# Performance work log

Measured on AMD Instinct MI355X. Metric: run time of the kernel, lower is better.

Reference implementation:

```python
import jax, jax.numpy as jnp
import numpy as np

B, N, E = 64, 20000, 160000
F_TEXT, HID, OUT = 300, 1024, 1664
NEG_SLOPE = 0.2


def setup_inputs() -> dict:
    key = jax.random.key(0)
    ks = jax.random.split(key, 9)
    img_feat = jax.random.normal(ks[0], (B, OUT), dtype=jnp.float32)
    node_features = jax.random.normal(ks[1], (N, F_TEXT), dtype=jnp.float32)
    edge_src = jax.random.randint(ks[2], (E,), 0, N, dtype=jnp.int32)
    edge_dst = jax.random.randint(ks[3], (E,), 0, N, dtype=jnp.int32)
    edge_weight = jax.random.uniform(ks[4], (E,), dtype=jnp.float32)
    W1 = jax.random.normal(ks[5], (F_TEXT, HID), dtype=jnp.float32) / np.sqrt(F_TEXT)
    b1 = jax.random.normal(ks[6], (HID,), dtype=jnp.float32) * 0.01
    W2 = jax.random.normal(ks[7], (HID, OUT), dtype=jnp.float32) / np.sqrt(HID)
    b2 = jax.random.normal(ks[8], (OUT,), dtype=jnp.float32) * 0.01
    return {"img_feat": img_feat, "node_features": node_features,
            "edge_src": edge_src, "edge_dst": edge_dst, "edge_weight": edge_weight,
            "W1": W1, "b1": b1, "W2": W2, "b2": b2}


def _gcn_norm(edge_src, edge_dst, edge_weight, num_nodes):
    # PyG gcn_norm with add_self_loops=False: symmetric degree normalization
    deg = jax.ops.segment_sum(edge_weight, edge_dst, num_segments=num_nodes)
    dinv = jnp.where(deg > 0, jax.lax.rsqrt(deg), 0.0)
    return dinv[edge_src] * edge_weight * dinv[edge_dst]


def _gcn_conv(x, edge_src, edge_dst, norm, W, b):
    # GCNConv: linear transform, then normalized gather -> scatter-add, then bias
    h = x @ W  # [N, out]
    msgs = h[edge_src] * norm[:, None]  # [E, out] gather + scale
    agg = jax.ops.segment_sum(msgs, edge_dst, num_segments=x.shape[0])
    return agg + b


def reference(img_feat, node_features, edge_src, edge_dst, edge_weight, W1, b1, W2, b2):
    num_nodes = node_features.shape[0]
    norm = _gcn_norm(edge_src, edge_dst, edge_weight, num_nodes)
    x = _gcn_conv(node_features, edge_src, edge_dst, norm, W1, b1)
    x = jnp.where(x >= 0, x, NEG_SLOPE * x)  # leaky_relu(0.2)
    x = _gcn_conv(x, edge_src, edge_dst, norm, W2, b2)
    return img_feat @ x.T  # [B, N]
```

## Files before the change

kernel.cpp:

```cpp
#include <hip/hip_runtime.h>
#include <hip/hip_bf16.h>

#define NNODES 20000
#define NEDGES 160000
#define BQ     64
#define FTEXT  300
#define KPAD1  320
#define HIDDIM 1024
#define OUTDIM 1664

typedef __attribute__((ext_vector_type(8))) short short8;
typedef __attribute__((ext_vector_type(4))) float floatx4;

__device__ inline unsigned short f2bf(float f) {
    union { float f; unsigned int u; } v; v.f = f;
    unsigned int r = v.u + 0x7FFF + ((v.u >> 16) & 1);
    return (unsigned short)(r >> 16);
}
__device__ inline float bf2f(unsigned short h) {
    union { unsigned int u; float f; } v; v.u = ((unsigned int)h) << 16;
    return v.f;
}

__global__ void degcnt_kernel(const int* __restrict__ dst, const float* __restrict__ w,
                              float* __restrict__ deg, int* __restrict__ cnt, int E) {
    int e = blockIdx.x * blockDim.x + threadIdx.x;
    if (e < E) {
        int d = dst[e];
        atomicAdd(&deg[d], w[e]);
        atomicAdd(&cnt[d], 1);
    }
}

__global__ __launch_bounds__(1024) void scan_kernel(const int* __restrict__ cnt,
                                                    int* __restrict__ row_start, int N) {
    __shared__ int partial[1024];
    const int CH = 20;
    int t = threadIdx.x;
    int begin = t * CH;
    int nloc = N - begin; if (nloc > CH) nloc = CH; if (nloc < 0) nloc = 0;
    int vals[CH];
    int s = 0;
    if (nloc == CH) {
        #pragma unroll
        for (int i = 0; i < CH / 4; i++) {
            int4 v = ((const int4*)(cnt + begin))[i];
            vals[i*4+0] = v.x; vals[i*4+1] = v.y; vals[i*4+2] = v.z; vals[i*4+3] = v.w;
            s += v.x + v.y + v.z + v.w;
        }
    } else {
        for (int i = 0; i < nloc; i++) { vals[i] = cnt[begin + i]; s += vals[i]; }
    }
    partial[t] = s;
    __syncthreads();
    for (int off = 1; off < 1024; off <<= 1) {
        int v = (t >= off) ? partial[t - off] : 0;
        __syncthreads();
        partial[t] += v;
        __syncthreads();
    }
    int run = (t == 0) ? 0 : partial[t - 1];
    for (int i = 0; i < nloc; i++) { row_start[begin + i] = run; run += vals[i]; }
    if (t == 1023) row_start[N] = partial[1023];
}

__global__ void fill_kernel(const int* __restrict__ dst, const int* __restrict__ src,
                            const float* __restrict__ w, const float* __restrict__ deg,
                            const int* __restrict__ row_start, int* __restrict__ cursor,
                            int* __restrict__ src_s, float* __restrict__ wnrm_s, int E) {
    int e = blockIdx.x * blockDim.x + threadIdx.x;
    if (e < E) {
        int d = dst[e], s = src[e];
        float dd = deg[d], ds = deg[s];
        float nv = (ds > 0.f ? rsqrtf(ds) : 0.f) * w[e] * (dd > 0.f ? rsqrtf(dd) : 0.f);
        int pos = row_start[d] + atomicAdd(&cursor[d], 1);
        src_s[pos] = s;
        wnrm_s[pos] = nv;
    }
}

__global__ __launch_bounds__(256) void aggnf_kernel(const unsigned short* __restrict__ nfb,
        const int* __restrict__ row_start, const int* __restrict__ src_s,
        const float* __restrict__ wnrm_s, unsigned short* __restrict__ out) {
    int wave = threadIdx.x >> 6, lane = threadIdx.x & 63;
    int d = blockIdx.x * 4 + wave;
    int s0 = row_start[d], s1 = row_start[d + 1];
    float4 acc  = make_float4(0.f, 0.f, 0.f, 0.f);
    float4 acc2 = make_float4(0.f, 0.f, 0.f, 0.f);
    for (int base = s0; base < s1; base += 64) {
        int m = s1 - base; if (m > 64) m = 64;
        int   src_l = (lane < m) ? src_s[base + lane]  : 0;
        float w_l   = (lane < m) ? wnrm_s[base + lane] : 0.f;
        int sj = __shfl(src_l, 0);
        float wj = __shfl(w_l, 0);
        const ushort4* row = (const ushort4*)(nfb + (long)sj * FTEXT);
        ushort4 hv  = row[lane];
        ushort4 hv2 = make_ushort4(0, 0, 0, 0);
        if (lane < 11) hv2 = row[64 + lane];
        for (int j = 0; j < m; j++) {
            ushort4 nv  = make_ushort4(0, 0, 0, 0);
            ushort4 nv2 = make_ushort4(0, 0, 0, 0);
            float wn = 0.f;
            if (j + 1 < m) {
                int sn = __shfl(src_l, j + 1);
                wn = __shfl(w_l, j + 1);
                const ushort4* nrow = (const ushort4*)(nfb + (long)sn * FTEXT);
                nv = nrow[lane];
                if (lane < 11) nv2 = nrow[64 + lane];
            }
            acc.x  += bf2f(hv.x)  * wj; acc.y  += bf2f(hv.y)  * wj;
            acc.z  += bf2f(hv.z)  * wj; acc.w  += bf2f(hv.w)  * wj;
            acc2.x += bf2f(hv2.x) * wj; acc2.y += bf2f(hv2.y) * wj;
            acc2.z += bf2f(hv2.z) * wj; acc2.w += bf2f(hv2.w) * wj;
            hv = nv; hv2 = nv2; wj = wn;
        }
    }
    unsigned short* orow = out + (long)d * KPAD1;
    ushort4 o;
    o.x = f2bf(acc.x); o.y = f2bf(acc.y); o.z = f2bf(acc.z); o.w = f2bf(acc.w);
    ((ushort4*)orow)[lane] = o;
    if (lane < 16) {
        ushort4 o2 = make_ushort4(0, 0, 0, 0);
        if (lane < 11) {
            o2.x = f2bf(acc2.x); o2.y = f2bf(acc2.y);
            o2.z = f2bf(acc2.z); o2.w = f2bf(acc2.w);
        }
        ((ushort4*)orow)[64 + lane] = o2;
    }
}

#define W1N  (HIDDIM * KPAD1)
#define N1F4 (HIDDIM * OUTDIM / 4)
#define N2F4 (BQ * OUTDIM / 4)
#define N3F4 (NNODES * FTEXT / 4)
__global__ void cvt_all_kernel(const float* __restrict__ W1, unsigned short* __restrict__ W1bt,
                               const float* __restrict__ W2, unsigned short* __restrict__ W2b,
                               const float* __restrict__ img, unsigned short* __restrict__ imgb,
                               const float* __restrict__ nf, unsigned short* __restrict__ nfb) {
    int i = blockIdx.x * 256 + threadIdx.x;
    if (i < W1N) {
        int n = i / KPAD1, k = i % KPAD1;
        float v = (k < FTEXT) ? W1[(long)k * HIDDIM + n] : 0.f;
        W1bt[i] = f2bf(v);
        return;
    }
    i -= W1N;
    const float* in; unsigned short* outp; int j;
    if (i < N1F4)                    { in = W2;  outp = W2b;  j = i; }
    else if (i < N1F4 + N2F4)        { in = img; outp = imgb; j = i - N1F4; }
    else if (i < N1F4 + N2F4 + N3F4) { in = nf;  outp = nfb;  j = i - N1F4 - N2F4; }
    else return;
    float4 v = ((const float4*)in)[j];
    ushort4 o;
    o.x = f2bf(v.x); o.y = f2bf(v.y); o.z = f2bf(v.z); o.w = f2bf(v.w);
    ((ushort4*)outp)[j] = o;
}

__global__ __launch_bounds__(256) void ztcvec_kernel(const float* __restrict__ Ztf,
        unsigned short* __restrict__ Zt, const float* __restrict__ img,
        const float* __restrict__ b2, float* __restrict__ cvec) {
    if (blockIdx.x < (BQ * HIDDIM) / 256) {
        int i = blockIdx.x * 256 + threadIdx.x;
        Zt[i] = f2bf(Ztf[i]);
    } else {
        int b = blockIdx.x - (BQ * HIDDIM) / 256;
        int l = threadIdx.x;
        float v = 0.f;
        for (int f = l; f < OUTDIM; f += 256) v += img[(long)b * OUTDIM + f] * b2[f];
        __shared__ float red[256];
        red[l] = v;
        __syncthreads();
        if (l < 64) {
            v = red[l] + red[l + 64] + red[l + 128] + red[l + 192];
            for (int off = 32; off > 0; off >>= 1) v += __shfl_down(v, off);
            if (l == 0) cvec[b] = v;
        }
    }
}

template<int EPI, int OUT_BF16, int ATOMIC, int NT>
__global__ __launch_bounds__(256) void mfma_gemm(
        const unsigned short* __restrict__ A, const unsigned short* __restrict__ B,
        const float* __restrict__ bias, void* __restrict__ Cv,
        int M, int N, int K, int ldc) {
    constexpr int CT = NT / 16;
    __shared__ unsigned short As[128][40];
    __shared__ unsigned short Bs[NT][40];
    int t = threadIdx.x;
    int m0 = blockIdx.y * 128;
    int n0 = blockIdx.x * NT;
    int klen = K / gridDim.z;
    int kbeg = blockIdx.z * klen;
    int wave = t >> 6, lane = t & 63;
    int lm = lane & 15, lq = lane >> 4;
    floatx4 acc[2][CT] = {};
    for (int k0 = kbeg; k0 < kbeg + klen; k0 += 32) {
        #pragma unroll
        for (int p = 0; p < 2; p++) {
            int idx = p * 256 + t;
            int r = idx >> 2, c8 = (idx & 3) * 8;
            uint4 v = make_uint4(0, 0, 0, 0);
            int gm = m0 + r;
            if (gm < M) v = *(const uint4*)(A + (long)gm * K + k0 + c8);
            *(uint4*)&As[r][c8] = v;
        }
        #pragma unroll
        for (int p = 0; p < NT / 64; p++) {
            int idx = p * 256 + t;
            int r = idx >> 2, c8 = (idx & 3) * 8;
            uint4 v = *(const uint4*)(B + (long)(n0 + r) * K + k0 + c8);
            *(uint4*)&Bs[r][c8] = v;
        }
        __syncthreads();
        short8 a[2], b[CT];
        #pragma unroll
        for (int rt = 0; rt < 2; rt++)
            a[rt] = *(const short8*)&As[wave * 32 + rt * 16 + lm][lq * 8];
        #pragma unroll
        for (int ct = 0; ct < CT; ct++)
            b[ct] = *(const short8*)&Bs[ct * 16 + lm][lq * 8];
        #pragma unroll
        for (int rt = 0; rt < 2; rt++)
            #pragma unroll
            for (int ct = 0; ct < CT; ct++)
                acc[rt][ct] = __builtin_amdgcn_mfma_f32_16x16x32_bf16(
                    a[rt], b[ct], acc[rt][ct], 0, 0, 0);
        __syncthreads();
    }
    #pragma unroll
    for (int rt = 0; rt < 2; rt++) {
        #pragma unroll
        for (int r = 0; r < 4; r++) {
            int gm = m0 + wave * 32 + rt * 16 + lq * 4 + r;
            if (gm >= M) continue;
            #pragma unroll
            for (int ct = 0; ct < CT; ct++) {
                int gn = n0 + ct * 16 + lm;
                float v = acc[rt][ct][r];
                if (EPI) { v += bias[gn]; v = v >= 0.f ? v : 0.2f * v; }
                if (OUT_BF16)      ((unsigned short*)Cv)[(long)gm * ldc + gn] = f2bf(v);
                else if (ATOMIC)   atomicAdd((float*)Cv + (long)gm * ldc + gn, v);
                else               ((float*)Cv)[(long)gm * ldc + gn] = v;
            }
        }
    }
}

__global__ __launch_bounds__(512) void xy_gemm(
        const unsigned short* __restrict__ aggNF, const unsigned short* __restrict__ W1bt,
        const float* __restrict__ b1, const unsigned short* __restrict__ Zt,
        float* __restrict__ Y, int M) {
    __shared__ unsigned short smem[128 * 136];
    unsigned short (*As)[40]  = (unsigned short (*)[40])smem;
    unsigned short (*Bs)[40]  = (unsigned short (*)[40])(smem + 5120);
    unsigned short (*xs)[136] = (unsigned short (*)[136])smem;
    int t = threadIdx.x;
    int wave = t >> 6, lane = t & 63;
    int lm = lane & 15, lq = lane >> 4;
    int m0 = blockIdx.y * 128;
    int n0 = blockIdx.x * 128;
    floatx4 acc[8] = {};
    for (int k0 = 0; k0 < KPAD1; k0 += 32) {
        {
            int r = t >> 2, c8 = (t & 3) * 8;
            uint4 v = make_uint4(0, 0, 0, 0);
            int gm = m0 + r;
            if (gm < M) v = *(const uint4*)(aggNF + (long)gm * KPAD1 + k0 + c8);
            *(uint4*)&As[r][c8] = v;
        }
        {
            int r = t >> 2, c8 = (t & 3) * 8;
            uint4 v = *(const uint4*)(W1bt + (long)(n0 + r) * KPAD1 + k0 + c8);
            *(uint4*)&Bs[r][c8] = v;
        }
        __syncthreads();
        short8 a = *(const short8*)&As[wave * 16 + lm][lq * 8];
        #pragma unroll
        for (int ct = 0; ct < 8; ct++) {
            short8 b = *(const short8*)&Bs[ct * 16 + lm][lq * 8];
            acc[ct] = __builtin_amdgcn_mfma_f32_16x16x32_bf16(a, b, acc[ct], 0, 0, 0);
        }
        __syncthreads();
    }
    #pragma unroll
    for (int ct = 0; ct < 8; ct++) {
        int col = ct * 16 + lm;
        float bv = b1[n0 + col];
        #pragma unroll
        for (int r = 0; r < 4; r++) {
            float v = acc[ct][r] + bv;
            v = v >= 0.f ? v : 0.2f * v;
            xs[wave * 16 + lq * 4 + r][col] = f2bf(v);
        }
    }
    __syncthreads();
    floatx4 yacc[4] = {};
    #pragma unroll
    for (int kk = 0; kk < 4; kk++) {
        short8 a = *(const short8*)&xs[wave * 16 + lm][kk * 32 + lq * 8];
        #pragma unroll
        for (int bt = 0; bt < 4; bt++) {
            short8 b = *(const short8*)(Zt + (long)(bt * 16 + lm) * HIDDIM
                                            + n0 + kk * 32 + lq * 8);
            yacc[bt] = __builtin_amdgcn_mfma_f32_16x16x32_bf16(a, b, yacc[bt], 0, 0, 0);
        }
    }
    #pragma unroll
    for (int bt = 0; bt < 4; bt++) {
        #pragma unroll
        for (int r = 0; r < 4; r++) {
            int gm = m0 + wave * 16 + lq * 4 + r;
            if (gm < M) atomicAdd(&Y[(long)gm * 64 + bt * 16 + lm], yacc[bt][r]);
        }
    }
}

__global__ __launch_bounds__(256) void outagg_kernel(const float* __restrict__ Y,
        const int* __restrict__ row_start, const int* __restrict__ src_s,
        const float* __restrict__ wnrm_s, const float* __restrict__ c,
        float* __restrict__ out, int N) {
    __shared__ float tile[4][68];
    int d0 = blockIdx.x * 4;
    int t = threadIdx.x;
    int wave = t >> 6, lane = t & 63;
    int d = d0 + wave;
    int s0 = row_start[d], s1 = row_start[d + 1];
    float acc = 0.f;
    for (int base = s0; base < s1; base += 64) {
        int m = s1 - base; if (m > 64) m = 64;
        int   src_l = (lane < m) ? src_s[base + lane]  : 0;
        float w_l   = (lane < m) ? wnrm_s[base + lane] : 0.f;
        int sj = __shfl(src_l, 0);
        float wj = __shfl(w_l, 0);
        float yv = Y[(long)sj * 64 + lane];
        for (int j = 0; j < m; j++) {
            float yn = 0.f, wn = 0.f;
            if (j + 1 < m) {
                int sn = __shfl(src_l, j + 1);
                wn = __shfl(w_l, j + 1);
                yn = Y[(long)sn * 64 + lane];
            }
            acc += wj * yv;
            yv = yn; wj = wn;
        }
    }
    tile[wave][lane] = acc + c[lane];
    __syncthreads();
    int b = t >> 2, j = t & 3;
    out[(long)b * N + d0 + j] = tile[j][b];
}

extern "C" void kernel_launch(void* const* d_in, const int* in_sizes, int n_in,
                              void* d_out, int out_size, void* d_ws, size_t ws_size,
                              hipStream_t stream) {
    const float* img_feat      = (const float*)d_in[0];
    const float* node_features = (const float*)d_in[1];
    const int*   edge_src      = (const int*)d_in[2];
    const int*   edge_dst      = (const int*)d_in[3];
    const float* edge_weight   = (const float*)d_in[4];
    const float* W1            = (const float*)d_in[5];
    const float* b1            = (const float*)d_in[6];
    const float* W2            = (const float*)d_in[7];
    const float* b2            = (const float*)d_in[8];
    float* out = (float*)d_out;

    const int N = NNODES, E = NEDGES;

    char* ws = (char*)d_ws;
    size_t off = 0;
    auto alloc = [&](size_t bytes) -> void* {
        void* p = ws + off;
        off = (off + bytes + 255) & ~(size_t)255;
        return p;
    };
    float*          deg       = (float*)alloc((size_t)N * 4);
    int*            cnt       = (int*)alloc((size_t)N * 4);
    int*            cursor    = (int*)alloc((size_t)N * 4);
    float*          Ztf       = (float*)alloc((size_t)BQ * HIDDIM * 4);
    float*          Y         = (float*)alloc((size_t)N * BQ * 4);
    size_t zero_bytes = off;
    int*            row_start = (int*)alloc((size_t)(N + 1) * 4);
    int*            src_s     = (int*)alloc((size_t)E * 4);
    float*          wnrm_s    = (float*)alloc((size_t)E * 4);
    unsigned short* aggNF     = (unsigned short*)alloc((size_t)N * KPAD1 * 2);
    unsigned short* W1bt      = (unsigned short*)alloc((size_t)HIDDIM * KPAD1 * 2);
    unsigned short* W2b       = (unsigned short*)alloc((size_t)HIDDIM * OUTDIM * 2);
    unsigned short* imgb      = (unsigned short*)alloc((size_t)BQ * OUTDIM * 2);
    unsigned short* nfb       = (unsigned short*)alloc((size_t)N * FTEXT * 2);
    unsigned short* Zt        = (unsigned short*)alloc((size_t)BQ * HIDDIM * 2);
    float*          cvec      = (float*)alloc((size_t)BQ * 4);

    hipMemsetAsync(ws, 0, zero_bytes, stream);

    int eb = (E + 255) / 256;
    degcnt_kernel<<<eb, 256, 0, stream>>>(edge_dst, edge_weight, deg, cnt, E);
    scan_kernel<<<1, 1024, 0, stream>>>(cnt, row_start, N);
    fill_kernel<<<eb, 256, 0, stream>>>(edge_dst, edge_src, edge_weight, deg, row_start,
                                        cursor, src_s, wnrm_s, E);

    cvt_all_kernel<<<(W1N + (N1F4 + N2F4 + N3F4) + 255) / 256, 256, 0, stream>>>(
        W1, W1bt, W2, W2b, img_feat, imgb, node_features, nfb);

    mfma_gemm<0, 0, 1, 64><<<dim3(HIDDIM / 64, 1, 13), 256, 0, stream>>>(
        imgb, W2b, nullptr, Ztf, BQ, HIDDIM, OUTDIM, HIDDIM);
    ztcvec_kernel<<<(BQ * HIDDIM) / 256 + BQ, 256, 0, stream>>>(Ztf, Zt, img_feat, b2, cvec);

    aggnf_kernel<<<N / 4, 256, 0, stream>>>(nfb, row_start, src_s, wnrm_s, aggNF);

    xy_gemm<<<dim3(HIDDIM / 128, (N + 127) / 128), 512, 0, stream>>>(
        aggNF, W1bt, b1, Zt, Y, N);

    outagg_kernel<<<N / 4, 256, 0, stream>>>(Y, row_start, src_s, wnrm_s, cvec, out, N);
}
```

Measured before the change: 243.3 us.

## Restructure fused X·W1·Zt GEMM to loop over all hidden tiles per row block

Each block now owns 80 rows of aggNF and walks all 1024 hidden columns in 128-wide chunks. A rows stay in registers, and a pre-chunked W1 layout is double-buffered into LDS via global_load_lds. Y is accumulated entirely in-block and written once, so the atomicAdds and the zeroing of Y are no longer needed. This removes the repeated A reloads across eight column blocks and the atomic traffic, in exchange for fewer blocks (250), a serial loop with a barrier per chunk, and higher register use.

```diff
diff --git a/kernel.cpp b/kernel.cpp
--- a/kernel.cpp
+++ b/kernel.cpp
@@ -20,6 +20,12 @@
 __device__ inline float bf2f(unsigned short h) {
     union { unsigned int u; float f; } v; v.u = ((unsigned int)h) << 16;
     return v.f;
+}
+
+__device__ inline void gload16(const unsigned short* g, unsigned short* l) {
+    __builtin_amdgcn_global_load_lds(
+        (const __attribute__((address_space(1))) unsigned int*)g,
+        (__attribute__((address_space(3))) unsigned int*)l, 16, 0, 0);
 }
 
 __global__ void degcnt_kernel(const int* __restrict__ dst, const float* __restrict__ w,
@@ -133,15 +139,22 @@
 #define N1F4 (HIDDIM * OUTDIM / 4)
 #define N2F4 (BQ * OUTDIM / 4)
 #define N3F4 (NNODES * FTEXT / 4)
-__global__ void cvt_all_kernel(const float* __restrict__ W1, unsigned short* __restrict__ W1bt,
+__global__ void cvt_all_kernel(const float* __restrict__ W1, unsigned short* __restrict__ W1ch,
                                const float* __restrict__ W2, unsigned short* __restrict__ W2b,
                                const float* __restrict__ img, unsigned short* __restrict__ imgb,
                                const float* __restrict__ nf, unsigned short* __restrict__ nfb) {
     int i = blockIdx.x * 256 + threadIdx.x;
     if (i < W1N) {
-        int n = i / KPAD1, k = i % KPAD1;
+        int c   = i >> 13;
+        int w   = i & 8191;
+        int h   = (w >> 12) & 1;
+        int lqg = (w >> 10) & 3;
+        int row = (w >> 3) & 127;
+        int j   = i & 7;
+        int n = (c / 5) * 128 + row;
+        int k = (c % 5) * 64 + h * 32 + lqg * 8 + j;
         float v = (k < FTEXT) ? W1[(long)k * HIDDIM + n] : 0.f;
-        W1bt[i] = f2bf(v);
+        W1ch[i] = f2bf(v);
         return;
     }
     i -= W1N;
@@ -246,72 +259,95 @@
     }
 }
 
-__global__ __launch_bounds__(512) void xy_gemm(
-        const unsigned short* __restrict__ aggNF, const unsigned short* __restrict__ W1bt,
+__global__ __launch_bounds__(640) void xy_gemm(
+        const unsigned short* __restrict__ aggNF, const unsigned short* __restrict__ W1ch,
         const float* __restrict__ b1, const unsigned short* __restrict__ Zt,
         float* __restrict__ Y, int M) {
-    __shared__ unsigned short smem[128 * 136];
-    unsigned short (*As)[40]  = (unsigned short (*)[40])smem;
-    unsigned short (*Bs)[40]  = (unsigned short (*)[40])(smem + 5120);
-    unsigned short (*xs)[136] = (unsigned short (*)[136])smem;
+    __shared__ unsigned short Bs[2][8192];
+    __shared__ unsigned short xs[80][136];
+    float (*ys)[68] = (float (*)[68])xs;
     int t = threadIdx.x;
     int wave = t >> 6, lane = t & 63;
     int lm = lane & 15, lq = lane >> 4;
-    int m0 = blockIdx.y * 128;
-    int n0 = blockIdx.x * 128;
-    floatx4 acc[8] = {};
-    for (int k0 = 0; k0 < KPAD1; k0 += 32) {
-        {
-            int r = t >> 2, c8 = (t & 3) * 8;
-            uint4 v = make_uint4(0, 0, 0, 0);
-            int gm = m0 + r;
-            if (gm < M) v = *(const uint4*)(aggNF + (long)gm * KPAD1 + k0 + c8);
-            *(uint4*)&As[r][c8] = v;
-        }
-        {
-            int r = t >> 2, c8 = (t & 3) * 8;
-            uint4 v = *(const uint4*)(W1bt + (long)(n0 + r) * KPAD1 + k0 + c8);
-            *(uint4*)&Bs[r][c8] = v;
-        }
-        __syncthreads();
-        short8 a = *(const short8*)&As[wave * 16 + lm][lq * 8];
-        #pragma unroll
-        for (int ct = 0; ct < 8; ct++) {
-            short8 b = *(const short8*)&Bs[ct * 16 + lm][lq * 8];
-            acc[ct] = __builtin_amdgcn_mfma_f32_16x16x32_bf16(a, b, acc[ct], 0, 0, 0);
-        }
-        __syncthreads();
-    }
-    #pragma unroll
-    for (int ct = 0; ct < 8; ct++) {
-        int col = ct * 16 + lm;
-        float bv = b1[n0 + col];
-        #pragma unroll
-        for (int r = 0; r < 4; r++) {
-            float v = acc[ct][r] + bv;
-            v = v >= 0.f ? v : 0.2f * v;
-            xs[wave * 16 + lq * 4 + r][col] = f2bf(v);
-        }
+    int wm = wave >> 1, wn = wave & 1;
+    int m0 = blockIdx.x * 80;
+
+    if (t < 512) {
+        gload16(W1ch + t * 8, &Bs[0][t * 8]);
+        gload16(W1ch + 4096 + t * 8, &Bs[0][4096 + t * 8]);
+    }
+    short8 afr[10];
+    {
+        const unsigned short* ap = aggNF + (long)(m0 + wm * 16 + lm) * KPAD1 + lq * 8;
+        #pragma unroll
+        for (int kk = 0; kk < 10; kk++)
+            afr[kk] = *(const short8*)(ap + kk * 32);
     }
     __syncthreads();
+    int cur = 0;
     floatx4 yacc[4] = {};
-    #pragma unroll
-    for (int kk = 0; kk < 4; kk++) {
-        short8 a = *(const short8*)&xs[wave * 16 + lm][kk * 32 + lq * 8];
-        #pragma unroll
-        for (int bt = 0; bt < 4; bt++) {
-            short8 b = *(const short8*)(Zt + (long)(bt * 16 + lm) * HIDDIM
-                                            + n0 + kk * 32 + lq * 8);
-            yacc[bt] = __builtin_amdgcn_mfma_f32_16x16x32_bf16(a, b, yacc[bt], 0, 0, 0);
-        }
-    }
-    #pragma unroll
-    for (int bt = 0; bt < 4; bt++) {
-        #pragma unroll
-        for (int r = 0; r < 4; r++) {
-            int gm = m0 + wave * 16 + lq * 4 + r;
-            if (gm < M) atomicAdd(&Y[(long)gm * 64 + bt * 16 + lm], yacc[bt][r]);
-        }
+    for (int nt = 0; nt < 8; nt++) {
+        floatx4 acc[4] = {};
+        for (int s = 0; s < 5; s++) {
+            int c = nt * 5 + s + 1;
+            if (c < 40 && t < 512) {
+                const unsigned short* src = W1ch + (long)c * 8192 + t * 8;
+                gload16(src,        &Bs[cur ^ 1][t * 8]);
+                gload16(src + 4096, &Bs[cur ^ 1][4096 + t * 8]);
+            }
+            #pragma unroll
+            for (int h = 0; h < 2; h++) {
+                short8 a = afr[s * 2 + h];
+                #pragma unroll
+                for (int ct = 0; ct < 4; ct++) {
+                    short8 b = *(const short8*)&Bs[cur][h * 4096 + lq * 1024
+                                                        + (wn * 64 + ct * 16 + lm) * 8];
+                    acc[ct] = __builtin_amdgcn_mfma_f32_16x16x32_bf16(a, b, acc[ct], 0, 0, 0);
+                }
+            }
+            __syncthreads();
+            cur ^= 1;
+        }
+        #pragma unroll
+        for (int ct = 0; ct < 4; ct++) {
+            int col = wn * 64 + ct * 16 + lm;
+            float bv = b1[nt * 128 + col];
+            #pragma unroll
+            for (int r = 0; r < 4; r++) {
+                float v = acc[ct][r] + bv;
+                v = v >= 0.f ? v : 0.2f * v;
+                xs[wm * 16 + lq * 4 + r][col] = f2bf(v);
+            }
+        }
+        #pragma unroll
+        for (int kk2 = 0; kk2 < 2; kk2++) {
+            short8 a = *(const short8*)&xs[wm * 16 + lm][wn * 64 + kk2 * 32 + lq * 8];
+            #pragma unroll
+            for (int bt = 0; bt < 4; bt++) {
+                short8 b = *(const short8*)(Zt + (long)(bt * 16 + lm) * HIDDIM
+                                                + nt * 128 + wn * 64 + kk2 * 32 + lq * 8);
+                yacc[bt] = __builtin_amdgcn_mfma_f32_16x16x32_bf16(a, b, yacc[bt], 0, 0, 0);
+            }
+        }
+    }
+    __syncthreads();
+    if (wn == 1) {
+        #pragma unroll
+        for (int bt = 0; bt < 4; bt++)
+            #pragma unroll
+            for (int r = 0; r < 4; r++)
+                ys[wm * 16 + lq * 4 + r][bt * 16 + lm] = yacc[bt][r];
+    }
+    __syncthreads();
+    if (wn == 0) {
+        #pragma unroll
+        for (int bt = 0; bt < 4; bt++)
+            #pragma unroll
+            for (int r = 0; r < 4; r++) {
+                int row = wm * 16 + lq * 4 + r;
+                Y[(long)(m0 + row) * 64 + bt * 16 + lm]
+                    = yacc[bt][r] + ys[row][bt * 16 + lm];
+            }
     }
 }
 
@@ -377,13 +413,13 @@
     int*            cnt       = (int*)alloc((size_t)N * 4);
     int*            cursor    = (int*)alloc((size_t)N * 4);
     float*          Ztf       = (float*)alloc((size_t)BQ * HIDDIM * 4);
+    size_t zero_bytes = off;
     float*          Y         = (float*)alloc((size_t)N * BQ * 4);
-    size_t zero_bytes = off;
     int*            row_start = (int*)alloc((size_t)(N + 1) * 4);
     int*            src_s     = (int*)alloc((size_t)E * 4);
     float*          wnrm_s    = (float*)alloc((size_t)E * 4);
     unsigned short* aggNF     = (unsigned short*)alloc((size_t)N * KPAD1 * 2);
-    unsigned short* W1bt      = (unsigned short*)alloc((size_t)HIDDIM * KPAD1 * 2);
+    unsigned short* W1ch      = (unsigned short*)alloc((size_t)HIDDIM * KPAD1 * 2);
     unsigned short* W2b       = (unsigned short*)alloc((size_t)HIDDIM * OUTDIM * 2);
     unsigned short* imgb      = (unsigned short*)alloc((size_t)BQ * OUTDIM * 2);
     unsigned short* nfb       = (unsigned short*)alloc((size_t)N * FTEXT * 2);
@@ -399,7 +435,7 @@
                                         cursor, src_s, wnrm_s, E);
 
     cvt_all_kernel<<<(W1N + (N1F4 + N2F4 + N3F4) + 255) / 256, 256, 0, stream>>>(
-        W1, W1bt, W2, W2b, img_feat, imgb, node_features, nfb);
+        W1, W1ch, W2, W2b, img_feat, imgb, node_features, nfb);
 
     mfma_gemm<0, 0, 1, 64><<<dim3(HIDDIM / 64, 1, 13), 256, 0, stream>>>(
         imgb, W2b, nullptr, Ztf, BQ, HIDDIM, OUTDIM, HIDDIM);
@@ -407,8 +443,7 @@
 
     aggnf_kernel<<<N / 4, 256, 0, stream>>>(nfb, row_start, src_s, wnrm_s, aggNF);
 
-    xy_gemm<<<dim3(HIDDIM / 128, (N + 127) / 128), 512, 0, stream>>>(
-        aggNF, W1bt, b1, Zt, Y, N);
+    xy_gemm<<<dim3(NNODES / 80), 640, 0, stream>>>(aggNF, W1ch, b1, Zt, Y, N);
 
     outagg_kernel<<<N / 4, 256, 0, stream>>>(Y, row_start, src_s, wnrm_s, cvec, out, N);
 }
```

Result: faster. 233.2 us (-4.2%).
